# Kernel optimization log

Hardware: AMD Instinct MI355X
Metric: run time of the kernel (lower is better)

The kernel has to match this reference:

```python
import jax, jax.numpy as jnp
import numpy as np

DM = 1024
H = 16
DEPTH = DM // H


def setup_inputs() -> dict:
    key = jax.random.key(0)
    ks = jax.random.split(key, 11)
    B, S = 2, 2048
    scale = 1.0 / np.sqrt(DM)
    inp = {
        "Q": jax.random.normal(ks[0], (B, S, DM), dtype=jnp.float32),
        "K": jax.random.normal(ks[1], (B, S, DM), dtype=jnp.float32),
        "V": jax.random.normal(ks[2], (B, S, DM), dtype=jnp.float32),
        "Wq": jax.random.normal(ks[3], (DM, DM), dtype=jnp.float32) * scale,
        "bq": jnp.zeros((DM,), dtype=jnp.float32),
        "Wk": jax.random.normal(ks[4], (DM, DM), dtype=jnp.float32) * scale,
        "bk": jnp.zeros((DM,), dtype=jnp.float32),
        "Wv": jax.random.normal(ks[5], (DM, DM), dtype=jnp.float32) * scale,
        "bv": jnp.zeros((DM,), dtype=jnp.float32),
        "Wo": jax.random.normal(ks[6], (DM, DM), dtype=jnp.float32) * scale,
        "bo": jnp.zeros((DM,), dtype=jnp.float32),
    }
    return inp


def _split_heads(x, B):
    # [B, S, DM] -> [B, H, S, DEPTH]
    return x.reshape(B, -1, H, DEPTH).transpose(0, 2, 1, 3)


def reference(Q, K, V, Wq, bq, Wk, bk, Wv, bv, Wo, bo):
    B = Q.shape[0]
    q = _split_heads(Q @ Wq + bq, B)  # [B,H,S,D]
    k = _split_heads(K @ Wk + bk, B)
    v = _split_heads(V @ Wv + bv, B)
    logits = jnp.einsum("bhqd,bhkd->bhqk", q, k) / jnp.sqrt(
        jnp.asarray(DEPTH, dtype=q.dtype))
    weights = jax.nn.softmax(logits, axis=-1)  # [B,H,S,S]
    attn = jnp.einsum("bhqk,bhkd->bhqd", weights, v)
    concat = attn.transpose(0, 2, 1, 3).reshape(B, -1, DM)
    output = concat @ Wo + bo
    return output, weights
```

## Files before the change

kernel.cpp:

```cpp
#include <hip/hip_runtime.h>
#include <hip/hip_fp16.h>
#include <stdint.h>
#include <stddef.h>

typedef _Float16 f16;
typedef _Float16 f16x8 __attribute__((ext_vector_type(8)));
typedef _Float16 f16x4 __attribute__((ext_vector_type(4)));
typedef float    f32x4 __attribute__((ext_vector_type(4)));

#define NB  2
#define NS  2048
#define NDM 1024
#define NH  16
#define ND  64
#define NM  4096

__global__ __launch_bounds__(256) void cvt_x_kernel(const float* __restrict__ q,
                                                    const float* __restrict__ k,
                                                    const float* __restrict__ v,
                                                    f16* __restrict__ xh)
{
    const float* src = (blockIdx.y == 0) ? q : (blockIdx.y == 1) ? k : v;
    f16* dst = xh + (size_t)blockIdx.y * ((size_t)NM * NDM);
    size_t i = ((size_t)blockIdx.x * 256 + threadIdx.x) * 8;
    float4 a = *(const float4*)(src + i);
    float4 b = *(const float4*)(src + i + 4);
    f16x8 o;
    o[0] = (f16)a.x; o[1] = (f16)a.y; o[2] = (f16)a.z; o[3] = (f16)a.w;
    o[4] = (f16)b.x; o[5] = (f16)b.y; o[6] = (f16)b.z; o[7] = (f16)b.w;
    *(f16x8*)(dst + i) = o;
}

__global__ __launch_bounds__(256) void transp_w_kernel(const float* __restrict__ w0,
                                                       const float* __restrict__ w1,
                                                       const float* __restrict__ w2,
                                                       const float* __restrict__ w3,
                                                       f16* __restrict__ wt)
{
    __shared__ float t[64][65];
    const int z = blockIdx.z;
    const float* src = (z==0)?w0:(z==1)?w1:(z==2)?w2:w3;
    f16* dst = wt + (size_t)z * ((size_t)NDM * NDM);
    const int k0 = blockIdx.y * 64, n0 = blockIdx.x * 64;
    const int c = threadIdx.x & 63, r4 = threadIdx.x >> 6;
    #pragma unroll
    for (int i = 0; i < 16; ++i) {
        int r = i*4 + r4;
        t[r][c] = src[(size_t)(k0 + r) * NDM + n0 + c];
    }
    __syncthreads();
    #pragma unroll
    for (int i = 0; i < 16; ++i) {
        int n = i*4 + r4;
        dst[(size_t)(n0 + n) * NDM + k0 + c] = (f16)t[c][n];
    }
}

template<int MODE>
__device__ __forceinline__ void gemm128(const f16* __restrict__ A,
                                        const f16* __restrict__ Bw,
                                        const float* __restrict__ bias,
                                        void* __restrict__ outp,
                                        f16* __restrict__ AsB, f16* __restrict__ BsB)
{
    const int tid  = threadIdx.x;
    const int lane = tid & 63;
    const int wid  = tid >> 6;
    const int wr = wid >> 1, wc = wid & 1;
    const int m0 = blockIdx.y * 128, n0 = blockIdx.x * 128;
    const int K = 1024;

    const int r0 = tid >> 2;
    const int s0 = (tid & 3) * 8;
    const f16* Arow0 = A  + (size_t)(m0 + r0)      * K + s0;
    const f16* Arow1 = A  + (size_t)(m0 + r0 + 64) * K + s0;
    const f16* Brow0 = Bw + (size_t)(n0 + r0)      * K + s0;
    const f16* Brow1 = Bw + (size_t)(n0 + r0 + 64) * K + s0;
    const int lds0 = r0*32 + s0;
    const int lds1 = (r0+64)*32 + s0;

    f16x8 ra0 = *(const f16x8*)(Arow0);
    f16x8 ra1 = *(const f16x8*)(Arow1);
    f16x8 rb0 = *(const f16x8*)(Brow0);
    f16x8 rb1 = *(const f16x8*)(Brow1);
    *(f16x8*)(AsB + lds0) = ra0; *(f16x8*)(AsB + lds1) = ra1;
    *(f16x8*)(BsB + lds0) = rb0; *(f16x8*)(BsB + lds1) = rb1;

    f32x4 acc[4][4];
    #pragma unroll
    for (int i = 0; i < 4; ++i)
        #pragma unroll
        for (int j = 0; j < 4; ++j) {
            f32x4 z4 = {0.f, 0.f, 0.f, 0.f};
            acc[i][j] = z4;
        }

    const int arow = wr*64 + (lane & 15);
    const int brow = wc*64 + (lane & 15);
    const int kc   = (lane >> 4) * 8;

    int cur = 0;
    for (int s = 0; s < 32; ++s) {
        const bool more = (s + 1 < 32);
        if (more) {
            const int kk = (s + 1) * 32;
            ra0 = *(const f16x8*)(Arow0 + kk); ra1 = *(const f16x8*)(Arow1 + kk);
            rb0 = *(const f16x8*)(Brow0 + kk); rb1 = *(const f16x8*)(Brow1 + kk);
        }
        __syncthreads();
        {
            f16x8 af[4], bf[4];
            f16* Asc = AsB + cur*4096;
            f16* Bsc = BsB + cur*4096;
            #pragma unroll
            for (int rt = 0; rt < 4; ++rt) af[rt] = *(const f16x8*)(Asc + (arow + rt*16)*32 + kc);
            #pragma unroll
            for (int ct = 0; ct < 4; ++ct) bf[ct] = *(const f16x8*)(Bsc + (brow + ct*16)*32 + kc);
            #pragma unroll
            for (int rt = 0; rt < 4; ++rt)
                #pragma unroll
                for (int ct = 0; ct < 4; ++ct)
                    acc[rt][ct] = __builtin_amdgcn_mfma_f32_16x16x32_f16(af[rt], bf[ct], acc[rt][ct], 0, 0, 0);
        }
        __syncthreads();
        if (more) {
            f16* Asn = AsB + (cur^1)*4096;
            f16* Bsn = BsB + (cur^1)*4096;
            *(f16x8*)(Asn + lds0) = ra0; *(f16x8*)(Asn + lds1) = ra1;
            *(f16x8*)(Bsn + lds0) = rb0; *(f16x8*)(Bsn + lds1) = rb1;
        }
        cur ^= 1;
    }

    #pragma unroll
    for (int rt = 0; rt < 4; ++rt) {
        const int mb = m0 + wr*64 + rt*16 + ((lane >> 4) << 2);
        #pragma unroll
        for (int ct = 0; ct < 4; ++ct) {
            const int n = n0 + wc*64 + ct*16 + (lane & 15);
            const float bn = bias[n];
            if (MODE == 0 || MODE == 1) {
                f16* dst = (f16*)outp;
                const float sc = (MODE == 0) ? 0.125f * 1.44269504088896f : 1.0f;
                #pragma unroll
                for (int j = 0; j < 4; ++j) {
                    const int m = mb + j;
                    const float v = (acc[rt][ct][j] + bn) * sc;
                    dst[(size_t)((m >> 11)*16 + (n >> 6))*131072 + (size_t)(m & 2047)*64 + (n & 63)] = (f16)v;
                }
            } else if (MODE == 2) {
                f16* dst = (f16*)outp;
                f16x4 o;
                #pragma unroll
                for (int j = 0; j < 4; ++j) o[j] = (f16)(acc[rt][ct][j] + bn);
                *(f16x4*)(dst + (size_t)((mb >> 11)*16 + (n >> 6))*131072 + (size_t)(n & 63)*2048 + (mb & 2047)) = o;
            } else {
                float* dst = (float*)outp;
                #pragma unroll
                for (int j = 0; j < 4; ++j) {
                    const int m = mb + j;
                    dst[(size_t)m * NDM + n] = acc[rt][ct][j] + bn;
                }
            }
        }
    }
}

__global__ __launch_bounds__(256) void proj_kernel(const f16* __restrict__ xh, const f16* __restrict__ wt,
                                                   const float* __restrict__ bq, const float* __restrict__ bk,
                                                   const float* __restrict__ bv,
                                                   f16* __restrict__ qh, f16* __restrict__ kh, f16* __restrict__ vh)
{
    __shared__ f16 AsS[2*4096];
    __shared__ f16 BsS[2*4096];
    const int z = blockIdx.z;
    const f16* A  = xh + (size_t)z * ((size_t)NM * NDM);
    const f16* Bw = wt + (size_t)z * ((size_t)NDM * NDM);
    if (z == 0)      gemm128<0>(A, Bw, bq, qh, AsS, BsS);
    else if (z == 1) gemm128<1>(A, Bw, bk, kh, AsS, BsS);
    else             gemm128<2>(A, Bw, bv, vh, AsS, BsS);
}

__global__ __launch_bounds__(256) void outproj_kernel(const f16* __restrict__ ah, const f16* __restrict__ wto,
                                                      const float* __restrict__ bo, float* __restrict__ out)
{
    __shared__ f16 AsS[2*4096];
    __shared__ f16 BsS[2*4096];
    gemm128<3>(ah, wto, bo, out, AsS, BsS);
}

__global__ __launch_bounds__(512) void attn_kernel(const f16* __restrict__ qh, const f16* __restrict__ kh,
                                                   const f16* __restrict__ vt, f16* __restrict__ ah,
                                                   float* __restrict__ wout)
{
    __shared__ f16   st[16 * 2056];
    __shared__ float redbuf[128];
    __shared__ float rinv[16];

    const int tid  = threadIdx.x;
    const int lane = tid & 63;
    const int wid  = tid >> 6;

    const int xcd   = blockIdx.x & 7;
    const int j     = blockIdx.x >> 3;
    const int bh    = xcd * 4 + (j & 3);
    const int qbase = (j >> 2) * 16;

    const f16* qp = qh + ((size_t)bh * NS + qbase) * 64;
    const f16* kp = kh + (size_t)bh * NS * 64;
    const f16* vp = vt + (size_t)bh * 64 * NS;

    const int l15 = lane & 15;
    const int g   = lane >> 4;

    const f16x8 qf0 = *(const f16x8*)(qp + l15*64 + g*8);
    const f16x8 qf1 = *(const f16x8*)(qp + l15*64 + 32 + g*8);

    float rs = 0.f;
    const f16* kbase = kp + (size_t)(wid*16 + l15) * 64 + g*8;
    f16* stw = st + l15*2056 + wid*16 + g*4;

    for (int t = 0; t < 16; ++t) {
        const f16* kb = kbase + (size_t)t * (128*64);
        f16x8 kf0 = *(const f16x8*)(kb);
        f16x8 kf1 = *(const f16x8*)(kb + 32);
        f32x4 a = {0.f, 0.f, 0.f, 0.f};
        a = __builtin_amdgcn_mfma_f32_16x16x32_f16(kf0, qf0, a, 0, 0, 0);
        a = __builtin_amdgcn_mfma_f32_16x16x32_f16(kf1, qf1, a, 0, 0, 0);
        f16x4 sv;
        #pragma unroll
        for (int u = 0; u < 4; ++u) {
            float e = __builtin_amdgcn_exp2f(a[u]);
            rs += e;
            sv[u] = (f16)e;
        }
        *(f16x4*)(stw + t*128) = sv;
    }

    rs += __shfl_xor(rs, 16);
    rs += __shfl_xor(rs, 32);
    if (lane < 16) redbuf[wid*16 + lane] = rs;
    __syncthreads();
    if (tid < 16) {
        float sum = 0.f;
        #pragma unroll
        for (int w = 0; w < 8; ++w) sum += redbuf[w*16 + tid];
        rinv[tid] = 1.0f / sum;
    }
    __syncthreads();

    if (wid < 4) {
        const int r = wid*4 + g;
        const float ri = rinv[r];
        const f16x4* srow = (const f16x4*)(st + r*2056);
        float* orow = wout + ((size_t)bh * NS + qbase + r) * NS;
        #pragma unroll 8
        for (int i = 0; i < 32; ++i) {
            f16x4 sv = srow[l15 + i*16];
            f32x4 o;
            o[0] = (float)sv[0] * ri; o[1] = (float)sv[1] * ri;
            o[2] = (float)sv[2] * ri; o[3] = (float)sv[3] * ri;
            __builtin_nontemporal_store(o, (f32x4*)(orow + (size_t)(l15 + i*16)*4));
        }
    } else {
        const int nt = wid - 4;
        f32x4 acc = {0.f, 0.f, 0.f, 0.f};
        const f16* vb = vp + (size_t)(nt*16 + l15) * NS + g*8;
        const f16* sb = st + l15*2056 + g*8;
        #pragma unroll 8
        for (int ks = 0; ks < 64; ++ks) {
            f16x8 vf = *(const f16x8*)(vb + ks*32);
            f16x8 sf = *(const f16x8*)(sb + ks*32);
            acc = __builtin_amdgcn_mfma_f32_16x16x32_f16(vf, sf, acc, 0, 0, 0);
        }
        const float ri = rinv[l15];
        const int bb = bh >> 4, hh = bh & 15;
        f16x4 o;
        #pragma unroll
        for (int u = 0; u < 4; ++u) o[u] = (f16)(acc[u] * ri);
        *(f16x4*)(ah + ((size_t)(bb*NS + qbase + l15)) * NDM + hh*64 + nt*16 + g*4) = o;
    }
}

extern "C" void kernel_launch(void* const* d_in, const int* in_sizes, int n_in,
                              void* d_out, int out_size, void* d_ws, size_t ws_size,
                              hipStream_t stream)
{
    (void)in_sizes; (void)n_in; (void)out_size;
    const float* Q  = (const float*)d_in[0];
    const float* K  = (const float*)d_in[1];
    const float* V  = (const float*)d_in[2];
    const float* Wq = (const float*)d_in[3];
    const float* bq = (const float*)d_in[4];
    const float* Wk = (const float*)d_in[5];
    const float* bk = (const float*)d_in[6];
    const float* Wv = (const float*)d_in[7];
    const float* bv = (const float*)d_in[8];
    const float* Wo = (const float*)d_in[9];
    const float* bo = (const float*)d_in[10];

    if (ws_size < 67108864ull) return;

    f16* ws = (f16*)d_ws;
    f16* Xh = ws;
    f16* Wt = ws + 12582912;
    f16* qh = ws + 16777216;
    f16* kh = ws + 20971520;
    f16* vt = ws + 25165824;
    f16* ah = ws + 29360128;
    float* out  = (float*)d_out;
    float* wout = out + 4194304;

    cvt_x_kernel  <<<dim3(2048, 3, 1), dim3(256), 0, stream>>>(Q, K, V, Xh);
    transp_w_kernel<<<dim3(16, 16, 4), dim3(256), 0, stream>>>(Wq, Wk, Wv, Wo, Wt);
    proj_kernel   <<<dim3(8, 32, 3),  dim3(256), 0, stream>>>(Xh, Wt, bq, bk, bv, qh, kh, vt);
    attn_kernel   <<<dim3(4096),      dim3(512), 0, stream>>>(qh, kh, vt, ah, wout);
    outproj_kernel<<<dim3(8, 32, 1),  dim3(256), 0, stream>>>(ah, Wt + 3*1048576, bo, out);
}
```

Before: 357.0 us.

## Keep attention probabilities in registers and split PV across all waves

The attention kernel no longer stages the full 16x2048 f16 probability tile in shared memory. Each wave keeps its exponentials in registers and writes the normalized weights straight to global memory. Every wave now runs a partial P·V product over its own key slice using 16x16x16 MFMAs, with V loads prefetched one step ahead. The eight partial results are then reduced through a small shared scratch buffer. This removes the large LDS buffer and the wave specialization between weight-writing and PV waves, in exchange for more registers, a cross-wave reduction, and smaller MFMA shapes.

```diff
diff --git a/kernel.cpp b/kernel.cpp
--- a/kernel.cpp
+++ b/kernel.cpp
@@ -193,13 +193,15 @@
                                                    const f16* __restrict__ vt, f16* __restrict__ ah,
                                                    float* __restrict__ wout)
 {
-    __shared__ f16   st[16 * 2056];
+    __shared__ __align__(16) float scratch[8][16][68];
     __shared__ float redbuf[128];
     __shared__ float rinv[16];
 
     const int tid  = threadIdx.x;
     const int lane = tid & 63;
     const int wid  = tid >> 6;
+    const int l15  = lane & 15;
+    const int g    = lane >> 4;
 
     const int xcd   = blockIdx.x & 7;
     const int j     = blockIdx.x >> 3;
@@ -210,31 +212,28 @@
     const f16* kp = kh + (size_t)bh * NS * 64;
     const f16* vp = vt + (size_t)bh * 64 * NS;
 
-    const int l15 = lane & 15;
-    const int g   = lane >> 4;
-
     const f16x8 qf0 = *(const f16x8*)(qp + l15*64 + g*8);
     const f16x8 qf1 = *(const f16x8*)(qp + l15*64 + 32 + g*8);
 
     float rs = 0.f;
+    f16x4 p16[16];
     const f16* kbase = kp + (size_t)(wid*16 + l15) * 64 + g*8;
-    f16* stw = st + l15*2056 + wid*16 + g*4;
-
+    #pragma unroll
     for (int t = 0; t < 16; ++t) {
-        const f16* kb = kbase + (size_t)t * (128*64);
+        const f16* kb = kbase + (size_t)t * 8192;
         f16x8 kf0 = *(const f16x8*)(kb);
         f16x8 kf1 = *(const f16x8*)(kb + 32);
         f32x4 a = {0.f, 0.f, 0.f, 0.f};
         a = __builtin_amdgcn_mfma_f32_16x16x32_f16(kf0, qf0, a, 0, 0, 0);
         a = __builtin_amdgcn_mfma_f32_16x16x32_f16(kf1, qf1, a, 0, 0, 0);
-        f16x4 sv;
+        f16x4 pv_;
         #pragma unroll
         for (int u = 0; u < 4; ++u) {
             float e = __builtin_amdgcn_exp2f(a[u]);
             rs += e;
-            sv[u] = (f16)e;
-        }
-        *(f16x4*)(stw + t*128) = sv;
+            pv_[u] = (f16)e;
+        }
+        p16[t] = pv_;
     }
 
     rs += __shfl_xor(rs, 16);
@@ -248,37 +247,60 @@
         rinv[tid] = 1.0f / sum;
     }
     __syncthreads();
-
-    if (wid < 4) {
-        const int r = wid*4 + g;
-        const float ri = rinv[r];
-        const f16x4* srow = (const f16x4*)(st + r*2056);
-        float* orow = wout + ((size_t)bh * NS + qbase + r) * NS;
-        #pragma unroll 8
-        for (int i = 0; i < 32; ++i) {
-            f16x4 sv = srow[l15 + i*16];
-            f32x4 o;
-            o[0] = (float)sv[0] * ri; o[1] = (float)sv[1] * ri;
-            o[2] = (float)sv[2] * ri; o[3] = (float)sv[3] * ri;
-            __builtin_nontemporal_store(o, (f32x4*)(orow + (size_t)(l15 + i*16)*4));
-        }
-    } else {
-        const int nt = wid - 4;
-        f32x4 acc = {0.f, 0.f, 0.f, 0.f};
-        const f16* vb = vp + (size_t)(nt*16 + l15) * NS + g*8;
-        const f16* sb = st + l15*2056 + g*8;
-        #pragma unroll 8
-        for (int ks = 0; ks < 64; ++ks) {
-            f16x8 vf = *(const f16x8*)(vb + ks*32);
-            f16x8 sf = *(const f16x8*)(sb + ks*32);
-            acc = __builtin_amdgcn_mfma_f32_16x16x32_f16(vf, sf, acc, 0, 0, 0);
-        }
-        const float ri = rinv[l15];
+    const float ri = rinv[l15];
+
+    const int kloc = wid*16 + g*4;
+    float* wr = wout + ((size_t)bh * NS + qbase + l15) * NS + kloc;
+    const f16* vb = vp + (size_t)l15 * NS + kloc;
+
+    f32x4 acc0 = {0.f,0.f,0.f,0.f}, acc1 = acc0, acc2 = acc0, acc3 = acc0;
+    f16x4 cV0 = *(const f16x4*)(vb);
+    f16x4 cV1 = *(const f16x4*)(vb + 16*NS);
+    f16x4 cV2 = *(const f16x4*)(vb + 32*NS);
+    f16x4 cV3 = *(const f16x4*)(vb + 48*NS);
+
+    #pragma unroll
+    for (int t = 0; t < 16; ++t) {
+        const int tn = (t + 1) & 15;
+        const f16* vn = vb + tn*128;
+        f16x4 nV0 = *(const f16x4*)(vn);
+        f16x4 nV1 = *(const f16x4*)(vn + 16*NS);
+        f16x4 nV2 = *(const f16x4*)(vn + 32*NS);
+        f16x4 nV3 = *(const f16x4*)(vn + 48*NS);
+
+        f32x4 w;
+        #pragma unroll
+        for (int u = 0; u < 4; ++u) w[u] = (float)p16[t][u] * ri;
+        __builtin_nontemporal_store(w, (f32x4*)(wr + t*128));
+
+        acc0 = __builtin_amdgcn_mfma_f32_16x16x16f16(cV0, p16[t], acc0, 0, 0, 0);
+        acc1 = __builtin_amdgcn_mfma_f32_16x16x16f16(cV1, p16[t], acc1, 0, 0, 0);
+        acc2 = __builtin_amdgcn_mfma_f32_16x16x16f16(cV2, p16[t], acc2, 0, 0, 0);
+        acc3 = __builtin_amdgcn_mfma_f32_16x16x16f16(cV3, p16[t], acc3, 0, 0, 0);
+
+        cV0 = nV0; cV1 = nV1; cV2 = nV2; cV3 = nV3;
+    }
+
+    {
+        float* sc = &scratch[wid][l15][g*4];
+        *(f32x4*)(sc)      = acc0;
+        *(f32x4*)(sc + 16) = acc1;
+        *(f32x4*)(sc + 32) = acc2;
+        *(f32x4*)(sc + 48) = acc3;
+    }
+    __syncthreads();
+
+    {
         const int bb = bh >> 4, hh = bh & 15;
-        f16x4 o;
-        #pragma unroll
-        for (int u = 0; u < 4; ++u) o[u] = (f16)(acc[u] * ri);
-        *(f16x4*)(ah + ((size_t)(bb*NS + qbase + l15)) * NDM + hh*64 + nt*16 + g*4) = o;
+        #pragma unroll
+        for (int r = 0; r < 2; ++r) {
+            const int idx = tid + r*512;
+            const int q = idx >> 6, d = idx & 63;
+            float s = 0.f;
+            #pragma unroll
+            for (int w2 = 0; w2 < 8; ++w2) s += scratch[w2][q][d];
+            ah[((size_t)(bb*NS + qbase + q)) * NDM + hh*64 + d] = (f16)(s * rinv[q]);
+        }
     }
 }
 
```

Measured after the change: 454.5 us. 27.3% more time.
